# Performance work log

Measured on AMD Instinct MI355X. Metric: run time of the kernel, lower is better.

The kernel has to match this reference:

```python
import jax, jax.numpy as jnp
import numpy as np

NEG_SLOPE = 0.01  # F.leaky_relu default


def gcn_layer(x, W, b, src, dst, n_nodes):
    """PyG GCNConv: out = D^-1/2 (A + I) D^-1/2 X W + b, edge_weight = 1."""
    E = src.shape[0]
    loops = jnp.arange(n_nodes, dtype=src.dtype)
    s = jnp.concatenate([src, loops])  # [E+N] sources incl. self-loops
    d = jnp.concatenate([dst, loops])  # [E+N] targets incl. self-loops
    deg = jax.ops.segment_sum(jnp.ones(E + n_nodes, x.dtype), d, num_segments=n_nodes)
    dinv = jnp.where(deg > 0, jax.lax.rsqrt(deg), 0.0)
    norm = dinv[s] * dinv[d]  # [E+N] symmetric normalization
    xw = x @ W  # [N, out] transform before aggregation (smaller gather)
    msg = xw[s] * norm[:, None]  # [E+N, out]
    out = jax.ops.segment_sum(msg, d, num_segments=n_nodes)  # scatter-add to targets
    return out + b


def setup_inputs() -> dict:
    key = jax.random.key(0)
    k1, k2, k3, k4 = jax.random.split(key, 4)
    N, E, nfeat, nhid = 50000, 800000, 128, 64
    x = jax.random.normal(k1, (N, nfeat), dtype=jnp.float32)
    edge_index = jax.random.randint(k2, (2, E), 0, N, dtype=jnp.int64)
    W1 = jax.random.normal(k3, (nfeat, nhid), dtype=jnp.float32) / np.sqrt(nfeat)
    b1 = jnp.zeros((nhid,), dtype=jnp.float32)
    W2 = jax.random.normal(k4, (nhid, nhid), dtype=jnp.float32) / np.sqrt(nhid)
    b2 = jnp.zeros((nhid,), dtype=jnp.float32)
    return {"x": x, "edge_index": edge_index, "W1": W1, "b1": b1, "W2": W2, "b2": b2}


def reference(x, edge_index, W1, b1, W2, b2):
    n_nodes = x.shape[0]
    src, dst = edge_index[0], edge_index[1]
    h = gcn_layer(x, W1, b1, src, dst, n_nodes)
    h = jax.nn.leaky_relu(h, NEG_SLOPE)
    out = gcn_layer(h, W2, b2, src, dst, n_nodes)
    return out
```

## Files before the change

kernel.cpp:

```cpp
#include <hip/hip_runtime.h>

#define NEG_SLOPE 0.01f

__device__ __forceinline__ void f4add(float4& a, const float4& v) {
    a.x += v.x; a.y += v.y; a.z += v.z; a.w += v.w;
}

__global__ __launch_bounds__(256) void k_zero(int* __restrict__ p, int n) {
    int i = blockIdx.x * 256 + threadIdx.x;
    if (i < n) p[i] = 0;
}

__global__ __launch_bounds__(256) void k_hist(const int* __restrict__ dst,
                                              int* __restrict__ cnt, int E) {
    int e = blockIdx.x * 256 + threadIdx.x;
    if (e < E) atomicAdd(&cnt[dst[e]], 1);
}

__global__ __launch_bounds__(256) void k_scan1(const int* __restrict__ cnt,
                                               int* __restrict__ incl,
                                               int* __restrict__ bsum,
                                               float* __restrict__ dinv, int n) {
    __shared__ int sm[256];
    int i = blockIdx.x * 256 + threadIdx.x;
    int t = threadIdx.x;
    int c = (i < n) ? cnt[i] : 0;
    if (i < n) dinv[i] = rsqrtf(1.0f + (float)c);
    sm[t] = c;
    __syncthreads();
    for (int ofs = 1; ofs < 256; ofs <<= 1) {
        int v = (t >= ofs) ? sm[t - ofs] : 0;
        __syncthreads();
        sm[t] += v;
        __syncthreads();
    }
    if (i < n) incl[i] = sm[t];
    if (t == 255) bsum[blockIdx.x] = sm[255];
}

__global__ __launch_bounds__(256) void k_scan2(int* __restrict__ bsum, int nb) {
    __shared__ int sm[256];
    int t = threadIdx.x;
    sm[t] = (t < nb) ? bsum[t] : 0;
    __syncthreads();
    for (int ofs = 1; ofs < 256; ofs <<= 1) {
        int v = (t >= ofs) ? sm[t - ofs] : 0;
        __syncthreads();
        sm[t] += v;
        __syncthreads();
    }
    if (t < nb) bsum[t] = sm[t];
}

__global__ __launch_bounds__(256) void k_scan3(const int* __restrict__ incl,
                                               const int* __restrict__ bsum,
                                               int* __restrict__ row_ptr,
                                               int* __restrict__ fill, int n) {
    int i = blockIdx.x * 256 + threadIdx.x;
    if (i < n) {
        int off = (blockIdx.x > 0) ? bsum[blockIdx.x - 1] : 0;
        row_ptr[i + 1] = incl[i] + off;
        fill[i] = 0;
    }
    if (i == 0) row_ptr[0] = 0;
}

__global__ __launch_bounds__(256) void k_gemm1_fill(
    const float* __restrict__ x, const float* __restrict__ W,
    const float* __restrict__ dinv, float* __restrict__ y, int n,
    const int* __restrict__ src, const int* __restrict__ dst,
    const int* __restrict__ row_ptr, int* __restrict__ fill,
    int* __restrict__ ssrc, int E, int nbe) {
    constexpr int K = 128;
    if ((int)blockIdx.x < nbe) {
        int e = blockIdx.x * 256 + threadIdx.x;
        if (e < E) {
            int d = dst[e];
            int pos = row_ptr[d] + atomicAdd(&fill[d], 1);
            ssrc[pos] = src[e];
        }
        return;
    }
    __shared__ float ws[K * 64];
    __shared__ float xs[32][K];
    const int tid = threadIdx.x;
    for (int t = tid; t < K * 16; t += 256)
        ((float4*)ws)[t] = ((const float4*)W)[t];
    const int row0 = (blockIdx.x - nbe) * 32;
    for (int t = tid; t < 8 * K; t += 256) {
        int r  = t / (K / 4);
        int kk = t - r * (K / 4);
        int row = row0 + r;
        float4 v = (row < n) ? ((const float4*)(x + (size_t)row * K))[kk]
                             : make_float4(0.f, 0.f, 0.f, 0.f);
        ((float4*)&xs[r][0])[kk] = v;
    }
    __syncthreads();
    const int wave  = tid >> 6;
    const int c     = tid & 63;
    const int rbase = wave * 8;
    float acc[8] = {};
#pragma unroll 4
    for (int k = 0; k < K; ++k) {
        float wv = ws[k * 64 + c];
#pragma unroll
        for (int r = 0; r < 8; ++r) acc[r] += xs[rbase + r][k] * wv;
    }
#pragma unroll
    for (int r = 0; r < 8; ++r) {
        int row = row0 + rbase + r;
        if (row < n) y[(size_t)row * 64 + c] = dinv[row] * acc[r];
    }
}

__global__ __launch_bounds__(256) void k_gemm64(const float* __restrict__ x,
                                                const float* __restrict__ W,
                                                const float* __restrict__ dinv,
                                                float* __restrict__ y, int n) {
    constexpr int K = 64;
    __shared__ float ws[K * 64];
    __shared__ float xs[32][K];
    const int tid = threadIdx.x;
    for (int t = tid; t < K * 16; t += 256)
        ((float4*)ws)[t] = ((const float4*)W)[t];
    const int row0 = blockIdx.x * 32;
    for (int t = tid; t < 8 * K; t += 256) {
        int r  = t / (K / 4);
        int kk = t - r * (K / 4);
        int row = row0 + r;
        float4 v = (row < n) ? ((const float4*)(x + (size_t)row * K))[kk]
                             : make_float4(0.f, 0.f, 0.f, 0.f);
        ((float4*)&xs[r][0])[kk] = v;
    }
    __syncthreads();
    const int wave  = tid >> 6;
    const int c     = tid & 63;
    const int rbase = wave * 8;
    float acc[8] = {};
#pragma unroll 4
    for (int k = 0; k < K; ++k) {
        float wv = ws[k * 64 + c];
#pragma unroll
        for (int r = 0; r < 8; ++r) acc[r] += xs[rbase + r][k] * wv;
    }
#pragma unroll
    for (int r = 0; r < 8; ++r) {
        int row = row0 + rbase + r;
        if (row < n) y[(size_t)row * 64 + c] = dinv[row] * acc[r];
    }
}

template <bool RELU>
__global__ __launch_bounds__(256) void k_gather(const int* __restrict__ row_ptr,
                                                const int* __restrict__ ssrc,
                                                const float* __restrict__ y,
                                                const float* __restrict__ dinv,
                                                const float* __restrict__ b,
                                                float* __restrict__ out, int n) {
    int node = blockIdx.x * 16 + (threadIdx.x >> 4);
    if (node >= n) return;
    int sub = threadIdx.x & 15;
    const float4* Y4 = (const float4*)y;
    float4 a0 = Y4[(size_t)node * 16 + sub];
    float4 a1 = make_float4(0.f, 0.f, 0.f, 0.f);
    float4 a2 = make_float4(0.f, 0.f, 0.f, 0.f);
    float4 a3 = make_float4(0.f, 0.f, 0.f, 0.f);
    int j = row_ptr[node];
    const int end = row_ptr[node + 1];
    for (; j + 4 <= end; j += 4) {
        int s0 = ssrc[j], s1 = ssrc[j + 1], s2 = ssrc[j + 2], s3 = ssrc[j + 3];
        float4 v0 = Y4[(size_t)s0 * 16 + sub];
        float4 v1 = Y4[(size_t)s1 * 16 + sub];
        float4 v2 = Y4[(size_t)s2 * 16 + sub];
        float4 v3 = Y4[(size_t)s3 * 16 + sub];
        f4add(a0, v0); f4add(a1, v1); f4add(a2, v2); f4add(a3, v3);
    }
    for (; j < end; ++j) {
        int s = ssrc[j];
        float4 v = Y4[(size_t)s * 16 + sub];
        f4add(a1, v);
    }
    f4add(a0, a1); f4add(a2, a3); f4add(a0, a2);
    float di = dinv[node];
    float4 bb = ((const float4*)b)[sub];
    float4 r;
    r.x = di * a0.x + bb.x;
    r.y = di * a0.y + bb.y;
    r.z = di * a0.z + bb.z;
    r.w = di * a0.w + bb.w;
    if (RELU) {
        r.x = (r.x > 0.f) ? r.x : NEG_SLOPE * r.x;
        r.y = (r.y > 0.f) ? r.y : NEG_SLOPE * r.y;
        r.z = (r.z > 0.f) ? r.z : NEG_SLOPE * r.z;
        r.w = (r.w > 0.f) ? r.w : NEG_SLOPE * r.w;
    }
    ((float4*)out)[(size_t)node * 16 + sub] = r;
}

extern "C" void kernel_launch(void* const* d_in, const int* in_sizes, int n_in,
                              void* d_out, int out_size, void* d_ws, size_t ws_size,
                              hipStream_t stream) {
    const float* x  = (const float*)d_in[0];
    const int*   ei = (const int*)d_in[1];
    const float* W1 = (const float*)d_in[2];
    const float* b1 = (const float*)d_in[3];
    const float* W2 = (const float*)d_in[4];
    const float* b2 = (const float*)d_in[5];
    float* out = (float*)d_out;

    const int N = in_sizes[0] / 128;
    const int E = in_sizes[1] / 2;
    const int* src = ei;
    const int* dst = ei + E;

    auto align = [](size_t v) { return (v + 255) & ~(size_t)255; };
    char* w = (char*)d_ws;
    size_t o = 0;
    int*   cnt     = (int*)(w + o);  o += align((size_t)N * 4);
    int*   fill    = (int*)(w + o);  o += align((size_t)N * 4);
    int*   incl    = (int*)(w + o);  o += align((size_t)N * 4);
    int*   bsum    = (int*)(w + o);  o += align(256 * 4);
    int*   row_ptr = (int*)(w + o);  o += align((size_t)(N + 1) * 4);
    float* dinv    = (float*)(w + o); o += align((size_t)N * 4);
    int*   ssrc    = (int*)(w + o);  o += align((size_t)E * 4);
    float* y       = (float*)(w + o); o += align((size_t)N * 64 * 4);
    float* h       = out;

    const int nb_n  = (N + 255) / 256;
    const int nb_e  = (E + 255) / 256;
    const int nb_g  = (N + 31) / 32;
    const int nb_a  = (N + 15) / 16;

    k_zero <<<nb_n, 256, 0, stream>>>(cnt, N);
    k_hist <<<nb_e, 256, 0, stream>>>(dst, cnt, E);
    k_scan1<<<nb_n, 256, 0, stream>>>(cnt, incl, bsum, dinv, N);
    k_scan2<<<1,    256, 0, stream>>>(bsum, nb_n);
    k_scan3<<<nb_n, 256, 0, stream>>>(incl, bsum, row_ptr, fill, N);

    k_gemm1_fill<<<nb_e + nb_g, 256, 0, stream>>>(x, W1, dinv, y, N,
                                                  src, dst, row_ptr, fill, ssrc, E, nb_e);
    k_gather<true><<<nb_a, 256, 0, stream>>>(row_ptr, ssrc, y, dinv, b1, h, N);

    k_gemm64<<<nb_g, 256, 0, stream>>>(h, W2, dinv, y, N);
    k_gather<false><<<nb_a, 256, 0, stream>>>(row_ptr, ssrc, y, dinv, b2, out, N);
}
```

Before: 263.5 us.

## Fuse layer-1 aggregation with layer-2 GEMM and tile GEMM over K chunks

Adds a kernel that aggregates neighbors for layer 1, applies bias and leaky ReLU into shared memory, and immediately multiplies by W2. This removes the round trip of h through global memory and one launch. The GEMM kernels now stage W and x in 32-wide K chunks, shrinking shared memory to raise occupancy, and gemm blocks are interleaved with CSR-fill blocks. The zero kernel is replaced with hipMemsetAsync. The fused path needs an extra N×64 workspace buffer, with a fallback if the workspace is too small.

```diff
diff --git a/kernel.cpp b/kernel.cpp
--- a/kernel.cpp
+++ b/kernel.cpp
@@ -4,11 +4,6 @@
 
 __device__ __forceinline__ void f4add(float4& a, const float4& v) {
     a.x += v.x; a.y += v.y; a.z += v.z; a.w += v.w;
-}
-
-__global__ __launch_bounds__(256) void k_zero(int* __restrict__ p, int n) {
-    int i = blockIdx.x * 256 + threadIdx.x;
-    if (i < n) p[i] = 0;
 }
 
 __global__ __launch_bounds__(256) void k_hist(const int* __restrict__ dst,
@@ -70,82 +65,87 @@
     const float* __restrict__ dinv, float* __restrict__ y, int n,
     const int* __restrict__ src, const int* __restrict__ dst,
     const int* __restrict__ row_ptr, int* __restrict__ fill,
-    int* __restrict__ ssrc, int E, int nbe) {
-    constexpr int K = 128;
-    if ((int)blockIdx.x < nbe) {
-        int e = blockIdx.x * 256 + threadIdx.x;
+    int* __restrict__ ssrc, int E, int nbg, int total) {
+    __shared__ float ws[32 * 64];
+    __shared__ float xs[32][32];
+    const int bid = blockIdx.x;
+    const int g  = (int)(((long long)bid * nbg) / total);
+    const int g1 = (int)(((long long)(bid + 1) * nbg) / total);
+    if (g1 == g) {
+        const int f = bid - g;
+        const int e = f * 256 + (int)threadIdx.x;
         if (e < E) {
-            int d = dst[e];
-            int pos = row_ptr[d] + atomicAdd(&fill[d], 1);
+            const int d = dst[e];
+            const int pos = row_ptr[d] + atomicAdd(&fill[d], 1);
             ssrc[pos] = src[e];
         }
         return;
     }
-    __shared__ float ws[K * 64];
-    __shared__ float xs[32][K];
     const int tid = threadIdx.x;
-    for (int t = tid; t < K * 16; t += 256)
-        ((float4*)ws)[t] = ((const float4*)W)[t];
-    const int row0 = (blockIdx.x - nbe) * 32;
-    for (int t = tid; t < 8 * K; t += 256) {
-        int r  = t / (K / 4);
-        int kk = t - r * (K / 4);
-        int row = row0 + r;
-        float4 v = (row < n) ? ((const float4*)(x + (size_t)row * K))[kk]
-                             : make_float4(0.f, 0.f, 0.f, 0.f);
-        ((float4*)&xs[r][0])[kk] = v;
-    }
-    __syncthreads();
-    const int wave  = tid >> 6;
-    const int c     = tid & 63;
-    const int rbase = wave * 8;
+    const int row0 = g * 32;
+    const int c = tid & 63;
+    const int rbase = (tid >> 6) * 8;
     float acc[8] = {};
-#pragma unroll 4
-    for (int k = 0; k < K; ++k) {
-        float wv = ws[k * 64 + c];
-#pragma unroll
-        for (int r = 0; r < 8; ++r) acc[r] += xs[rbase + r][k] * wv;
+    for (int kc = 0; kc < 128; kc += 32) {
+        for (int t = tid; t < 512; t += 256)
+            ((float4*)ws)[t] = ((const float4*)(W + (size_t)kc * 64))[t];
+        {
+            const int r = tid >> 3, kk = tid & 7;
+            const int row = row0 + r;
+            float4 v = (row < n) ? ((const float4*)(x + (size_t)row * 128 + kc))[kk]
+                                 : make_float4(0.f, 0.f, 0.f, 0.f);
+            ((float4*)&xs[r][0])[kk] = v;
+        }
+        __syncthreads();
+#pragma unroll
+        for (int k = 0; k < 32; ++k) {
+            const float wv = ws[k * 64 + c];
+#pragma unroll
+            for (int r = 0; r < 8; ++r) acc[r] += xs[rbase + r][k] * wv;
+        }
+        __syncthreads();
     }
 #pragma unroll
     for (int r = 0; r < 8; ++r) {
-        int row = row0 + rbase + r;
+        const int row = row0 + rbase + r;
         if (row < n) y[(size_t)row * 64 + c] = dinv[row] * acc[r];
     }
 }
 
-__global__ __launch_bounds__(256) void k_gemm64(const float* __restrict__ x,
-                                                const float* __restrict__ W,
-                                                const float* __restrict__ dinv,
-                                                float* __restrict__ y, int n) {
-    constexpr int K = 64;
-    __shared__ float ws[K * 64];
-    __shared__ float xs[32][K];
+template <int K>
+__global__ __launch_bounds__(256) void k_gemm(const float* __restrict__ x,
+                                              const float* __restrict__ W,
+                                              const float* __restrict__ dinv,
+                                              float* __restrict__ y, int n) {
+    __shared__ float ws[32 * 64];
+    __shared__ float xs[32][32];
     const int tid = threadIdx.x;
-    for (int t = tid; t < K * 16; t += 256)
-        ((float4*)ws)[t] = ((const float4*)W)[t];
     const int row0 = blockIdx.x * 32;
-    for (int t = tid; t < 8 * K; t += 256) {
-        int r  = t / (K / 4);
-        int kk = t - r * (K / 4);
-        int row = row0 + r;
-        float4 v = (row < n) ? ((const float4*)(x + (size_t)row * K))[kk]
-                             : make_float4(0.f, 0.f, 0.f, 0.f);
-        ((float4*)&xs[r][0])[kk] = v;
-    }
-    __syncthreads();
-    const int wave  = tid >> 6;
-    const int c     = tid & 63;
-    const int rbase = wave * 8;
+    const int c = tid & 63;
+    const int rbase = (tid >> 6) * 8;
     float acc[8] = {};
-#pragma unroll 4
-    for (int k = 0; k < K; ++k) {
-        float wv = ws[k * 64 + c];
-#pragma unroll
-        for (int r = 0; r < 8; ++r) acc[r] += xs[rbase + r][k] * wv;
+    for (int kc = 0; kc < K; kc += 32) {
+        for (int t = tid; t < 512; t += 256)
+            ((float4*)ws)[t] = ((const float4*)(W + (size_t)kc * 64))[t];
+        {
+            const int r = tid >> 3, kk = tid & 7;
+            const int row = row0 + r;
+            float4 v = (row < n) ? ((const float4*)(x + (size_t)row * K + kc))[kk]
+                                 : make_float4(0.f, 0.f, 0.f, 0.f);
+            ((float4*)&xs[r][0])[kk] = v;
+        }
+        __syncthreads();
+#pragma unroll
+        for (int k = 0; k < 32; ++k) {
+            const float wv = ws[k * 64 + c];
+#pragma unroll
+            for (int r = 0; r < 8; ++r) acc[r] += xs[rbase + r][k] * wv;
+        }
+        __syncthreads();
     }
 #pragma unroll
     for (int r = 0; r < 8; ++r) {
-        int row = row0 + rbase + r;
+        const int row = row0 + rbase + r;
         if (row < n) y[(size_t)row * 64 + c] = dinv[row] * acc[r];
     }
 }
@@ -197,6 +197,77 @@
     ((float4*)out)[(size_t)node * 16 + sub] = r;
 }
 
+__global__ __launch_bounds__(256) void k_gather_gemm(
+    const int* __restrict__ row_ptr, const int* __restrict__ ssrc,
+    const float* __restrict__ y, const float* __restrict__ dinv,
+    const float* __restrict__ b1, const float* __restrict__ W2,
+    float* __restrict__ y2, int n) {
+    __shared__ float hs[32][64];
+    __shared__ float ws[32 * 64];
+    const int tid = threadIdx.x;
+    const int row0 = blockIdx.x * 32;
+    const int qw = tid >> 4, sub = tid & 15;
+    const float4* Y4 = (const float4*)y;
+    const float4 bb = ((const float4*)b1)[sub];
+#pragma unroll
+    for (int half = 0; half < 2; ++half) {
+        const int node = row0 + half * 16 + qw;
+        if (node < n) {
+            float4 a0 = Y4[(size_t)node * 16 + sub];
+            float4 a1 = make_float4(0.f, 0.f, 0.f, 0.f);
+            float4 a2 = make_float4(0.f, 0.f, 0.f, 0.f);
+            float4 a3 = make_float4(0.f, 0.f, 0.f, 0.f);
+            int j = row_ptr[node];
+            const int end = row_ptr[node + 1];
+            for (; j + 4 <= end; j += 4) {
+                int s0 = ssrc[j], s1 = ssrc[j + 1], s2 = ssrc[j + 2], s3 = ssrc[j + 3];
+                float4 v0 = Y4[(size_t)s0 * 16 + sub];
+                float4 v1 = Y4[(size_t)s1 * 16 + sub];
+                float4 v2 = Y4[(size_t)s2 * 16 + sub];
+                float4 v3 = Y4[(size_t)s3 * 16 + sub];
+                f4add(a0, v0); f4add(a1, v1); f4add(a2, v2); f4add(a3, v3);
+            }
+            for (; j < end; ++j) {
+                int s = ssrc[j];
+                float4 v = Y4[(size_t)s * 16 + sub];
+                f4add(a1, v);
+            }
+            f4add(a0, a1); f4add(a2, a3); f4add(a0, a2);
+            const float di = dinv[node];
+            float4 r;
+            r.x = di * a0.x + bb.x;
+            r.y = di * a0.y + bb.y;
+            r.z = di * a0.z + bb.z;
+            r.w = di * a0.w + bb.w;
+            r.x = (r.x > 0.f) ? r.x : NEG_SLOPE * r.x;
+            r.y = (r.y > 0.f) ? r.y : NEG_SLOPE * r.y;
+            r.z = (r.z > 0.f) ? r.z : NEG_SLOPE * r.z;
+            r.w = (r.w > 0.f) ? r.w : NEG_SLOPE * r.w;
+            ((float4*)&hs[half * 16 + qw][0])[sub] = r;
+        }
+    }
+    const int c = tid & 63;
+    const int rbase = (tid >> 6) * 8;
+    float acc[8] = {};
+    for (int kc = 0; kc < 64; kc += 32) {
+        for (int t = tid; t < 512; t += 256)
+            ((float4*)ws)[t] = ((const float4*)(W2 + (size_t)kc * 64))[t];
+        __syncthreads();
+#pragma unroll
+        for (int k = 0; k < 32; ++k) {
+            const float wv = ws[k * 64 + c];
+#pragma unroll
+            for (int r = 0; r < 8; ++r) acc[r] += hs[rbase + r][kc + k] * wv;
+        }
+        __syncthreads();
+    }
+#pragma unroll
+    for (int r = 0; r < 8; ++r) {
+        const int row = row0 + rbase + r;
+        if (row < n) y2[(size_t)row * 64 + c] = dinv[row] * acc[r];
+    }
+}
+
 extern "C" void kernel_launch(void* const* d_in, const int* in_sizes, int n_in,
                               void* d_out, int out_size, void* d_ws, size_t ws_size,
                               hipStream_t stream) {
@@ -224,23 +295,30 @@
     float* dinv    = (float*)(w + o); o += align((size_t)N * 4);
     int*   ssrc    = (int*)(w + o);  o += align((size_t)E * 4);
     float* y       = (float*)(w + o); o += align((size_t)N * 64 * 4);
-    float* h       = out;
-
-    const int nb_n  = (N + 255) / 256;
-    const int nb_e  = (E + 255) / 256;
-    const int nb_g  = (N + 31) / 32;
-    const int nb_a  = (N + 15) / 16;
-
-    k_zero <<<nb_n, 256, 0, stream>>>(cnt, N);
+    float* y2      = (float*)(w + o); o += align((size_t)N * 64 * 4);
+    const bool have_y2 = (o <= ws_size);
+
+    const int nb_n = (N + 255) / 256;
+    const int nb_e = (E + 255) / 256;
+    const int nb_g = (N + 31) / 32;
+    const int nb_a = (N + 15) / 16;
+
+    hipMemsetAsync(cnt, 0, (size_t)N * 4, stream);
     k_hist <<<nb_e, 256, 0, stream>>>(dst, cnt, E);
     k_scan1<<<nb_n, 256, 0, stream>>>(cnt, incl, bsum, dinv, N);
     k_scan2<<<1,    256, 0, stream>>>(bsum, nb_n);
     k_scan3<<<nb_n, 256, 0, stream>>>(incl, bsum, row_ptr, fill, N);
 
     k_gemm1_fill<<<nb_e + nb_g, 256, 0, stream>>>(x, W1, dinv, y, N,
-                                                  src, dst, row_ptr, fill, ssrc, E, nb_e);
-    k_gather<true><<<nb_a, 256, 0, stream>>>(row_ptr, ssrc, y, dinv, b1, h, N);
-
-    k_gemm64<<<nb_g, 256, 0, stream>>>(h, W2, dinv, y, N);
-    k_gather<false><<<nb_a, 256, 0, stream>>>(row_ptr, ssrc, y, dinv, b2, out, N);
-}
+                                                  src, dst, row_ptr, fill, ssrc,
+                                                  E, nb_g, nb_e + nb_g);
+
+    if (have_y2) {
+        k_gather_gemm<<<nb_g, 256, 0, stream>>>(row_ptr, ssrc, y, dinv, b1, W2, y2, N);
+        k_gather<false><<<nb_a, 256, 0, stream>>>(row_ptr, ssrc, y2, dinv, b2, out, N);
+    } else {
+        k_gather<true><<<nb_a, 256, 0, stream>>>(row_ptr, ssrc, y, dinv, b1, out, N);
+        k_gemm<64><<<nb_g, 256, 0, stream>>>(out, W2, dinv, y, N);
+        k_gather<false><<<nb_a, 256, 0, stream>>>(row_ptr, ssrc, y, dinv, b2, out, N);
+    }
+}
```

Measured after the change: 307.8 us. +16.8%, slower.
